# Kernel optimization log

Measured on AMD Instinct MI355X. Metric: run time of the kernel, lower is better.

Reference implementation:

```python
import jax, jax.numpy as jnp
import numpy as np

B, S, E, H, NQ = 8, 2048, 8, 2, 8
D = E // H  # head_dim = 4
DIM = 2 ** NQ  # 256-amplitude state vector

# CNOT chain pattern from the module: (0,1),(1,2),...,(NQ-2,NQ-1),(NQ-1,0)
CNOTS = [(i, i + 1) for i in range(NQ - 1)] + [(NQ - 1, 0)]

# Pauli-Z sign table: wire 0 is the most-significant qubit axis (torchquantum convention)
_k = np.arange(DIM)
_SIGNS = (1.0 - 2.0 * ((_k[None, :] >> (NQ - 1 - np.arange(NQ))[:, None]) & 1)).astype(np.float32)  # (NQ, DIM)


def _quantum_measure(tok):
    """Batched simulation of the per-token circuit. tok: (N, E) real -> (N, NQ) <Z> values."""
    n = tok.shape[0]
    idx = jnp.arange(NQ) % D
    # encoder RX(tok[w]) then explicit RX(tok[w % head_dim]) on each wire: angles add.
    half = 0.5 * (tok[:, :NQ] + tok[:, idx])  # (N, NQ)
    a0 = jnp.cos(half).astype(jnp.complex64)
    a1 = (-1j) * jnp.sin(half).astype(jnp.complex64)
    qub = jnp.stack([a0, a1], axis=-1)  # (N, NQ, 2) per-qubit states (product state before CNOTs)
    # Kronecker product across the fixed NQ wires
    state = qub[:, 0, :]
    for w in range(1, NQ):
        state = (state[:, :, None] * qub[:, w, None, :]).reshape(n, -1)
    state = state.reshape((n,) + (2,) * NQ)
    # CNOT chain: flip target axis within control=1 block
    for c, t in CNOTS:
        c0 = jax.lax.index_in_dim(state, 0, c + 1, keepdims=True)
        c1 = jnp.flip(jax.lax.index_in_dim(state, 1, c + 1, keepdims=True), axis=t + 1)
        state = jnp.concatenate([c0, c1], axis=c + 1)
    p = (state.real ** 2 + state.imag ** 2).reshape(n, DIM)  # probabilities
    return p @ jnp.asarray(_SIGNS.T)  # (N, NQ) Pauli-Z expectations


def setup_inputs() -> dict:
    key = jax.random.key(0)
    ks = jax.random.split(key, 5)
    sc = 1.0 / np.sqrt(E)
    return {
        "x": jax.random.normal(ks[0], (B, S, E), jnp.float32),
        "Wq": jax.random.normal(ks[1], (E, E), jnp.float32) * sc,
        "Wk": jax.random.normal(ks[2], (E, E), jnp.float32) * sc,
        "Wv": jax.random.normal(ks[3], (E, E), jnp.float32) * sc,
        "Wo": jax.random.normal(ks[4], (E, E), jnp.float32) * sc,
    }


def reference(x, Wq, Wk, Wv, Wo):
    b, s, _ = x.shape
    # nn.Linear(bias=False): y = x @ W^T
    q = jnp.einsum('bse,fe->bsf', x, Wq).reshape(b, s, H, D)
    k = jnp.einsum('bse,fe->bsf', x, Wk).reshape(b, s, H, D)
    v = jnp.einsum('bse,fe->bsf', x, Wv).reshape(b, s, H, D)
    scores = jnp.einsum('bihd,bjhd->bhij', q, k) / jnp.sqrt(jnp.float32(D))
    attn = jax.nn.softmax(scores, axis=-1)  # dropout is identity at inference
    out = jnp.einsum('bhij,bjhd->bihd', attn, v).reshape(b, s, E)
    z = _quantum_measure(out.reshape(-1, E)).reshape(b, s, NQ)  # NQ == E
    return jnp.einsum('bsq,fq->bsf', z, Wo)
```

## Files before the change

kernel.cpp:

```cpp
#include <hip/hip_runtime.h>


#define SS 2048
#define EE 8

extern "C" __global__ __launch_bounds__(256, 8)
void qa_attn9(const float* __restrict__ x, const float* __restrict__ Wq,
              const float* __restrict__ Wk, const float* __restrict__ Wv,
              float* __restrict__ wsD, float4* __restrict__ wsA) {
    __shared__ float wrow[96];
    __shared__ __align__(16) float4 kv4[512];
    __shared__ float rden[3 * 128];
    __shared__ __align__(16) float4 racc[3 * 128];

    const int bid = blockIdx.x;
    const int jw = bid & 7, rt = (bid >> 3) & 15, h = (bid >> 7) & 1, b = bid >> 8;
    const int tid = threadIdx.x, lane = tid & 63, w = tid >> 6;

    if (tid < 96) {
        const int grp = tid >> 5, d = (tid >> 3) & 3, e = tid & 7;
        const float* W = (grp == 0) ? Wq : (grp == 1 ? Wk : Wv);
        float val = W[(h * 4 + d) * EE + e];
        if (grp == 0) val *= 0.72134752044f;
        wrow[tid] = val;
    }
    __syncthreads();

    {
        const int j = jw * 256 + tid;
        const float* xp = x + ((size_t)(b * SS + j)) * EE;
        float xv[8];
        *(float4*)&xv[0] = *(const float4*)xp;
        *(float4*)&xv[4] = *(const float4*)(xp + 4);
        float kk[4], vv[4];
        #pragma unroll
        for (int d = 0; d < 4; ++d) {
            float sk = 0.f, sv = 0.f;
            #pragma unroll
            for (int e = 0; e < 8; ++e) {
                sk += xv[e] * wrow[32 + d * 8 + e];
                sv += xv[e] * wrow[64 + d * 8 + e];
            }
            kk[d] = sk; vv[d] = sv;
        }
        kv4[tid * 2]     = make_float4(kk[0], kk[1], kk[2], kk[3]);
        kv4[tid * 2 + 1] = make_float4(vv[0], vv[1], vv[2], vv[3]);
    }

    float q[2][4];
    const int row0 = rt * 128 + lane;
    #pragma unroll
    for (int m = 0; m < 2; ++m) {
        const float* xp = x + ((size_t)(b * SS + row0 + m * 64)) * EE;
        float xv[8];
        *(float4*)&xv[0] = *(const float4*)xp;
        *(float4*)&xv[4] = *(const float4*)(xp + 4);
        #pragma unroll
        for (int d = 0; d < 4; ++d) {
            float s = 0.f;
            #pragma unroll
            for (int e = 0; e < 8; ++e) s += xv[e] * wrow[d * 8 + e];
            q[m][d] = s;
        }
    }
    __syncthreads();

    float den[2] = {};
    float acc[2][4] = {};
    const float4* kvp = &kv4[w * 128];
    #pragma unroll 2
    for (int jl = 0; jl < 64; ++jl) {
        const float4 kk = kvp[jl * 2];
        const float4 vv = kvp[jl * 2 + 1];
        #pragma unroll
        for (int m = 0; m < 2; ++m) {
            const float s = q[m][0] * kk.x + q[m][1] * kk.y
                          + q[m][2] * kk.z + q[m][3] * kk.w;
            const float e = __builtin_amdgcn_exp2f(s);
            den[m] += e;
            acc[m][0] += e * vv.x; acc[m][1] += e * vv.y;
            acc[m][2] += e * vv.z; acc[m][3] += e * vv.w;
        }
    }

    if (w > 0) {
        #pragma unroll
        for (int m = 0; m < 2; ++m) {
            rden[(w - 1) * 128 + lane + m * 64] = den[m];
            racc[(w - 1) * 128 + lane + m * 64] =
                make_float4(acc[m][0], acc[m][1], acc[m][2], acc[m][3]);
        }
    }
    __syncthreads();
    if (w == 0) {
        #pragma unroll
        for (int m = 0; m < 2; ++m) {
            const int r = lane + m * 64;
            float d = den[m] + rden[r] + rden[128 + r] + rden[256 + r];
            float4 a1 = racc[r], a2 = racc[128 + r], a3 = racc[256 + r];
            float4 a = make_float4(acc[m][0] + a1.x + a2.x + a3.x,
                                   acc[m][1] + a1.y + a2.y + a3.y,
                                   acc[m][2] + a1.z + a2.z + a3.z,
                                   acc[m][3] + a1.w + a2.w + a3.w);
            const size_t idx = ((size_t)((b * 2 + h) * 8 + jw)) * SS + row0 + m * 64;
            wsD[idx] = d;
            wsA[idx] = a;
        }
    }
}

extern "C" __global__ __launch_bounds__(256)
void qa_merge9(const float* __restrict__ wsD, const float4* __restrict__ wsA,
               const float* __restrict__ Wo, float* __restrict__ out) {
    __shared__ float wo[64];
    const int tid = threadIdx.x;
    if (tid < 64) wo[tid] = Wo[tid];
    __syncthreads();

    const int gt = blockIdx.x * 256 + tid;
    const int g = gt >> 1, h = gt & 1;
    const int b = g >> 11, s = g & 2047;

    float den = 0.f, a0 = 0.f, a1 = 0.f, a2 = 0.f, a3 = 0.f;
    #pragma unroll
    for (int sl = 0; sl < 8; ++sl) {
        const size_t idx = ((size_t)((b * 2 + h) * 8 + sl)) * SS + s;
        den += wsD[idx];
        const float4 p = wsA[idx];
        a0 += p.x; a1 += p.y; a2 += p.z; a3 += p.w;
    }
    const float inv = 1.f / den;
    float own[4] = {a0 * inv, a1 * inv, a2 * inv, a3 * inv};
    float oth[4];
    #pragma unroll
    for (int c = 0; c < 4; ++c) oth[c] = __shfl_xor(own[c], 1);

    float tok[8];
    #pragma unroll
    for (int c = 0; c < 4; ++c) {
        tok[c]     = h ? oth[c] : own[c];
        tok[4 + c] = h ? own[c] : oth[c];
    }

    float cc[8];
    #pragma unroll
    for (int ww = 0; ww < 8; ++ww) cc[ww] = __cosf(tok[ww] + tok[ww & 3]);

    float z[8];
    float p = 1.f;
    #pragma unroll
    for (int qq = 1; qq < 8; ++qq) { p *= cc[qq]; z[qq] = p; }
    z[0] = p;
    #pragma unroll
    for (int qq = 1; qq < 8; ++qq) z[qq] *= cc[0];

    float y[4];
    #pragma unroll
    for (int f = 0; f < 4; ++f) {
        float sum = 0.f;
        #pragma unroll
        for (int qq = 0; qq < 8; ++qq) sum += z[qq] * wo[(h * 4 + f) * 8 + qq];
        y[f] = sum;
    }
    float4* op = (float4*)(out + (size_t)g * 8) + h;
    *op = make_float4(y[0], y[1], y[2], y[3]);
}

extern "C" void kernel_launch(void* const* d_in, const int* in_sizes, int n_in,
                              void* d_out, int out_size, void* d_ws, size_t ws_size,
                              hipStream_t stream) {
    const float* x  = (const float*)d_in[0];
    const float* Wq = (const float*)d_in[1];
    const float* Wk = (const float*)d_in[2];
    const float* Wv = (const float*)d_in[3];
    const float* Wo = (const float*)d_in[4];
    float* out = (float*)d_out;

    float*  wsD = (float*)d_ws;
    float4* wsA = (float4*)((char*)d_ws + (16 * 8 * 2048) * sizeof(float));

    qa_attn9<<<dim3(2048), dim3(256), 0, stream>>>(x, Wq, Wk, Wv, wsD, wsA);
    qa_merge9<<<dim3(128), dim3(256), 0, stream>>>(wsD, wsA, Wo, out);
}
```

Before: 86.62 us.

## Retile attention blocks to 256 query rows by 128 keys, alias shared memory

Each block now handles 256 query rows (4 per thread) against 128 keys instead of 128 rows against 256 keys. This doubles the number of key splits to 16 and the size of the merge workspace. The K/V projection is split across thread pairs, and the reduction buffers share memory with the KV tile behind an added barrier. The aim is more register-level reuse of each K/V value loaded from LDS. In exchange, the merge kernel has twice as many partials to read and registers per thread go up.

```diff
diff --git a/kernel.cpp b/kernel.cpp
--- a/kernel.cpp
+++ b/kernel.cpp
@@ -5,16 +5,17 @@
 #define EE 8
 
 extern "C" __global__ __launch_bounds__(256, 8)
-void qa_attn9(const float* __restrict__ x, const float* __restrict__ Wq,
-              const float* __restrict__ Wk, const float* __restrict__ Wv,
-              float* __restrict__ wsD, float4* __restrict__ wsA) {
+void qa_attn10(const float* __restrict__ x, const float* __restrict__ Wq,
+               const float* __restrict__ Wk, const float* __restrict__ Wv,
+               float* __restrict__ wsD, float4* __restrict__ wsA) {
     __shared__ float wrow[96];
-    __shared__ __align__(16) float4 kv4[512];
-    __shared__ float rden[3 * 128];
-    __shared__ __align__(16) float4 racc[3 * 128];
+    __shared__ __align__(16) unsigned char smem[15360];
+    float4* kv4  = (float4*)smem;
+    float*  rden = (float*)smem;
+    float4* racc = (float4*)(smem + 3072);
 
     const int bid = blockIdx.x;
-    const int jw = bid & 7, rt = (bid >> 3) & 15, h = (bid >> 7) & 1, b = bid >> 8;
+    const int jw = bid & 15, rt = (bid >> 4) & 7, h = (bid >> 7) & 1, b = bid >> 8;
     const int tid = threadIdx.x, lane = tid & 63, w = tid >> 6;
 
     if (tid < 96) {
@@ -27,30 +28,28 @@
     __syncthreads();
 
     {
-        const int j = jw * 256 + tid;
+        const int jloc = tid >> 1, half = tid & 1;
+        const int j = jw * 128 + jloc;
         const float* xp = x + ((size_t)(b * SS + j)) * EE;
         float xv[8];
         *(float4*)&xv[0] = *(const float4*)xp;
         *(float4*)&xv[4] = *(const float4*)(xp + 4);
-        float kk[4], vv[4];
+        const float* wsel = wrow + 32 + half * 32;
+        float o[4];
         #pragma unroll
         for (int d = 0; d < 4; ++d) {
-            float sk = 0.f, sv = 0.f;
+            float s = 0.f;
             #pragma unroll
-            for (int e = 0; e < 8; ++e) {
-                sk += xv[e] * wrow[32 + d * 8 + e];
-                sv += xv[e] * wrow[64 + d * 8 + e];
-            }
-            kk[d] = sk; vv[d] = sv;
+            for (int e = 0; e < 8; ++e) s += xv[e] * wsel[d * 8 + e];
+            o[d] = s;
         }
-        kv4[tid * 2]     = make_float4(kk[0], kk[1], kk[2], kk[3]);
-        kv4[tid * 2 + 1] = make_float4(vv[0], vv[1], vv[2], vv[3]);
+        kv4[jloc * 2 + half] = make_float4(o[0], o[1], o[2], o[3]);
     }
 
-    float q[2][4];
-    const int row0 = rt * 128 + lane;
+    float q[4][4];
+    const int row0 = rt * 256 + lane;
     #pragma unroll
-    for (int m = 0; m < 2; ++m) {
+    for (int m = 0; m < 4; ++m) {
         const float* xp = x + ((size_t)(b * SS + row0 + m * 64)) * EE;
         float xv[8];
         *(float4*)&xv[0] = *(const float4*)xp;
@@ -65,15 +64,15 @@
     }
     __syncthreads();
 
-    float den[2] = {};
-    float acc[2][4] = {};
-    const float4* kvp = &kv4[w * 128];
+    float den[4] = {};
+    float acc[4][4] = {};
+    const float4* kvp = &kv4[w * 64];
     #pragma unroll 2
-    for (int jl = 0; jl < 64; ++jl) {
+    for (int jl = 0; jl < 32; ++jl) {
         const float4 kk = kvp[jl * 2];
         const float4 vv = kvp[jl * 2 + 1];
         #pragma unroll
-        for (int m = 0; m < 2; ++m) {
+        for (int m = 0; m < 4; ++m) {
             const float s = q[m][0] * kk.x + q[m][1] * kk.y
                           + q[m][2] * kk.z + q[m][3] * kk.w;
             const float e = __builtin_amdgcn_exp2f(s);
@@ -82,27 +81,28 @@
             acc[m][2] += e * vv.z; acc[m][3] += e * vv.w;
         }
     }
+    __syncthreads();
 
     if (w > 0) {
         #pragma unroll
-        for (int m = 0; m < 2; ++m) {
-            rden[(w - 1) * 128 + lane + m * 64] = den[m];
-            racc[(w - 1) * 128 + lane + m * 64] =
+        for (int m = 0; m < 4; ++m) {
+            rden[(w - 1) * 256 + lane + m * 64] = den[m];
+            racc[(w - 1) * 256 + lane + m * 64] =
                 make_float4(acc[m][0], acc[m][1], acc[m][2], acc[m][3]);
         }
     }
     __syncthreads();
     if (w == 0) {
         #pragma unroll
-        for (int m = 0; m < 2; ++m) {
+        for (int m = 0; m < 4; ++m) {
             const int r = lane + m * 64;
-            float d = den[m] + rden[r] + rden[128 + r] + rden[256 + r];
-            float4 a1 = racc[r], a2 = racc[128 + r], a3 = racc[256 + r];
+            float d = den[m] + rden[r] + rden[256 + r] + rden[512 + r];
+            float4 a1 = racc[r], a2 = racc[256 + r], a3 = racc[512 + r];
             float4 a = make_float4(acc[m][0] + a1.x + a2.x + a3.x,
                                    acc[m][1] + a1.y + a2.y + a3.y,
                                    acc[m][2] + a1.z + a2.z + a3.z,
                                    acc[m][3] + a1.w + a2.w + a3.w);
-            const size_t idx = ((size_t)((b * 2 + h) * 8 + jw)) * SS + row0 + m * 64;
+            const size_t idx = ((size_t)((b * 2 + h) * 16 + jw)) * SS + row0 + m * 64;
             wsD[idx] = d;
             wsA[idx] = a;
         }
@@ -110,8 +110,8 @@
 }
 
 extern "C" __global__ __launch_bounds__(256)
-void qa_merge9(const float* __restrict__ wsD, const float4* __restrict__ wsA,
-               const float* __restrict__ Wo, float* __restrict__ out) {
+void qa_merge10(const float* __restrict__ wsD, const float4* __restrict__ wsA,
+                const float* __restrict__ Wo, float* __restrict__ out) {
     __shared__ float wo[64];
     const int tid = threadIdx.x;
     if (tid < 64) wo[tid] = Wo[tid];
@@ -123,8 +123,8 @@
 
     float den = 0.f, a0 = 0.f, a1 = 0.f, a2 = 0.f, a3 = 0.f;
     #pragma unroll
-    for (int sl = 0; sl < 8; ++sl) {
-        const size_t idx = ((size_t)((b * 2 + h) * 8 + sl)) * SS + s;
+    for (int sl = 0; sl < 16; ++sl) {
+        const size_t idx = ((size_t)((b * 2 + h) * 16 + sl)) * SS + s;
         den += wsD[idx];
         const float4 p = wsA[idx];
         a0 += p.x; a1 += p.y; a2 += p.z; a3 += p.w;
@@ -177,8 +177,8 @@
     float* out = (float*)d_out;
 
     float*  wsD = (float*)d_ws;
-    float4* wsA = (float4*)((char*)d_ws + (16 * 8 * 2048) * sizeof(float));
+    float4* wsA = (float4*)((char*)d_ws + (16 * 16 * 2048) * sizeof(float));
 
-    qa_attn9<<<dim3(2048), dim3(256), 0, stream>>>(x, Wq, Wk, Wv, wsD, wsA);
-    qa_merge9<<<dim3(128), dim3(256), 0, stream>>>(wsD, wsA, Wo, out);
+    qa_attn10<<<dim3(2048), dim3(256), 0, stream>>>(x, Wq, Wk, Wv, wsD, wsA);
+    qa_merge10<<<dim3(128), dim3(256), 0, stream>>>(wsD, wsA, Wo, out);
 }
```

After: 96.22 us. 1.11x slower.
